# Optimization experiments

Measured on AMD Instinct MI355X. Metric: run time of the kernel, lower is better.

## Reference

```python
import jax, jax.numpy as jnp
import numpy as np

H = 1024
B, S = 8, 2048

def setup_inputs() -> dict:
    key = jax.random.key(0)
    ks = jax.random.split(key, 7)
    inputs = jax.random.normal(ks[0], (B, S, H), dtype=jnp.float32)
    mask = jnp.ones((B, S), dtype=jnp.int32)
    sc = 1.0 / np.sqrt(H)
    Wq = jax.random.normal(ks[1], (H, H), dtype=jnp.float32) * sc
    bq = jnp.zeros((H,), dtype=jnp.float32)
    Wk = jax.random.normal(ks[2], (H, H), dtype=jnp.float32) * sc
    bk = jnp.zeros((H,), dtype=jnp.float32)
    Wv = jax.random.normal(ks[3], (H, H), dtype=jnp.float32) * sc
    bv = jnp.zeros((H,), dtype=jnp.float32)
    return {"inputs": inputs, "mask": mask, "Wq": Wq, "bq": bq, "Wk": Wk, "bk": bk, "Wv": Wv, "bv": bv}

def reference(inputs, mask, Wq, bq, Wk, bk, Wv, bv):
    scale = jnp.asarray(H ** 0.5, inputs.dtype)
    q = jnp.einsum('bsh,hd->bsd', inputs, Wq) + bq
    k = jnp.einsum('bsh,hd->bsd', inputs, Wk) + bk
    v = jnp.einsum('bsh,hd->bsd', inputs, Wv) + bv
    scores = jnp.einsum('bqd,bkd->bqk', q, k) / scale  # [B,S,S]
    scores = jnp.where(mask[:, None, :] == 0, -jnp.inf, scores)
    attn = jax.nn.softmax(scores, axis=-1)
    return jnp.einsum('bqk,bkd->bqd', attn, v)
```

## Files before the change

kernel.cpp:

```cpp
#include <hip/hip_runtime.h>
#include <stdint.h>

#define DEVI __device__ __forceinline__

typedef __bf16 bf16x8 __attribute__((ext_vector_type(8)));
typedef float  floatx4 __attribute__((ext_vector_type(4)));


DEVI unsigned short f2bf(float f) {
  union { float f; uint32_t u; } x; x.f = f;
  return (unsigned short)((x.u + 0x7fffu + ((x.u >> 16) & 1u)) >> 16);
}
DEVI float bf2f(unsigned short s) {
  union { uint32_t u; float f; } x; x.u = ((uint32_t)s) << 16;
  return x.f;
}

__global__ __launch_bounds__(256) void k_prep(
    const float* __restrict__ X, unsigned short* __restrict__ Xb,
    const float* __restrict__ Wq, const float* __restrict__ Wk,
    const float* __restrict__ Wv, unsigned short* __restrict__ Wt,
    float* __restrict__ lvec) {
  __shared__ float tile[64][65];
  int bx = blockIdx.x, t = threadIdx.x;
  if (bx < 16384) {
    int i = bx * 256 + t;
    float4 v = ((const float4*)X)[i];
    ushort4 o;
    o.x = f2bf(v.x); o.y = f2bf(v.y); o.z = f2bf(v.z); o.w = f2bf(v.w);
    ((ushort4*)Xb)[i] = o;
  } else if (bx < 17152) {
    int idx = bx - 16384;
    int sel = idx >> 8, b2 = idx & 255;
    const float* W = sel == 0 ? Wq : (sel == 1 ? Wk : Wv);
    unsigned short* Wo = Wt + ((size_t)sel << 20);
    int h0 = (b2 & 15) * 64, d0 = (b2 >> 4) * 64;
#pragma unroll
    for (int i = 0; i < 16; ++i) {
      int idx2 = i * 256 + t; int r = idx2 >> 6, c = idx2 & 63;
      tile[r][c] = W[(size_t)(h0 + r) * 1024 + d0 + c];
    }
    __syncthreads();
#pragma unroll
    for (int i = 0; i < 16; ++i) {
      int idx2 = i * 256 + t; int r = idx2 >> 6, c = idx2 & 63;
      Wo[(size_t)(d0 + r) * 1024 + h0 + c] = f2bf(tile[c][r]);
    }
  } else {
    float4 z4 = {0.f, 0.f, 0.f, 0.f};
#pragma unroll
    for (int i = 0; i < 16; ++i) ((float4*)lvec)[i * 256 + t] = z4;
  }
}

DEVI void gl_lds16(const unsigned short* gp, unsigned short* lp) {
  __builtin_amdgcn_global_load_lds(
      (const __attribute__((address_space(1))) void*)gp,
      (__attribute__((address_space(3))) void*)lp, 16, 0, 0);
}

template <int EPI>
__global__ __launch_bounds__(256) void k_gemm(
    const unsigned short* __restrict__ A, const unsigned short* __restrict__ Bt,
    void* __restrict__ Cv,
    const float* __restrict__ bias_q, const float* __restrict__ bias_k,
    const float* __restrict__ bias_v,
    const float* __restrict__ lvec, float* __restrict__ lsum,
    const int* __restrict__ mask,
    long aZ, long bZ, int ldA, int ldB, int kIters)
{
  __shared__ unsigned short As[128 * 64];
  __shared__ unsigned short Bs[128 * 64];
  const int t = threadIdx.x, w = t >> 6, l = t & 63;
  const int quad = l >> 4, l15 = l & 15;
  const int m0 = blockIdx.x * 128;
  const int z = blockIdx.z;
  const int wm = (w & 1) * 64, wn = (w >> 1) * 64;

  int n0, sel = 0;
  if constexpr (EPI == 4) { sel = blockIdx.y >> 3; n0 = (blockIdx.y & 7) * 128; }
  else n0 = blockIdx.y * 128;

  const unsigned short* Az = A + (size_t)z * aZ;
  const unsigned short* Bz = (EPI == 4) ? (Bt + ((size_t)sel << 20))
                                        : (Bt + (size_t)z * bZ);

  floatx4 acc[4][4];
#pragma unroll
  for (int i = 0; i < 4; ++i)
#pragma unroll
    for (int j = 0; j < 4; ++j) { floatx4 zz = {0.f, 0.f, 0.f, 0.f}; acc[i][j] = zz; }

  for (int kt = 0; kt < kIters; ++kt) {
    __syncthreads();
#pragma unroll
    for (int i = 0; i < 4; ++i) {
      int u   = (i * 4 + w) * 64 + l;
      int row = u >> 3;
      int cc  = (u & 7) ^ (row & 7);
      gl_lds16(Az + (size_t)(m0 + row) * ldA + kt * 64 + cc * 8,
               &As[(i * 4 + w) * 512]);
      gl_lds16(Bz + (size_t)(n0 + row) * ldB + kt * 64 + cc * 8,
               &Bs[(i * 4 + w) * 512]);
    }
    __syncthreads();
#pragma unroll
    for (int ks = 0; ks < 2; ++ks) {
      bf16x8 af[4], bfr[4];
#pragma unroll
      for (int ms = 0; ms < 4; ++ms) {
        int r  = wm + ms * 16 + l15;
        int cc = (ks * 4 + quad) ^ (r & 7);
        af[ms] = *(const bf16x8*)&As[r * 64 + cc * 8];
      }
#pragma unroll
      for (int ns = 0; ns < 4; ++ns) {
        int r  = wn + ns * 16 + l15;
        int cc = (ks * 4 + quad) ^ (r & 7);
        bfr[ns] = *(const bf16x8*)&Bs[r * 64 + cc * 8];
      }
#pragma unroll
      for (int ms = 0; ms < 4; ++ms)
#pragma unroll
        for (int ns = 0; ns < 4; ++ns)
          acc[ms][ns] = __builtin_amdgcn_mfma_f32_16x16x32_bf16(
              af[ms], bfr[ns], acc[ms][ns], 0, 0, 0);
    }
  }

  if constexpr (EPI == 4) {
    unsigned short* C = (unsigned short*)Cv + ((size_t)sel << 24);
    const float* bs = sel == 0 ? bias_q : (sel == 1 ? bias_k : bias_v);
    if (sel < 2) {
      float sc = sel == 0 ? 0.03125f : 1.0f;
#pragma unroll
      for (int ns = 0; ns < 4; ++ns) {
        int n_g = n0 + wn + ns * 16 + l15;
        float bv = bs[n_g];
#pragma unroll
        for (int ms = 0; ms < 4; ++ms) {
          int mb = m0 + wm + ms * 16 + quad * 4;
#pragma unroll
          for (int r = 0; r < 4; ++r)
            C[(size_t)(mb + r) * 1024 + n_g] = f2bf((acc[ms][ns][r] + bv) * sc);
        }
      }
    } else {
#pragma unroll
      for (int ns = 0; ns < 4; ++ns) {
        int n_g = n0 + wn + ns * 16 + l15;
        float bv = bs[n_g];
#pragma unroll
        for (int ms = 0; ms < 4; ++ms) {
          int m_g = m0 + wm + ms * 16 + quad * 4;
          int bb = m_g >> 11, key = m_g & 2047;
          ushort4 pk;
          pk.x = f2bf(acc[ms][ns][0] + bv);
          pk.y = f2bf(acc[ms][ns][1] + bv);
          pk.z = f2bf(acc[ms][ns][2] + bv);
          pk.w = f2bf(acc[ms][ns][3] + bv);
          *(ushort4*)&C[((size_t)bb << 21) + ((size_t)n_g << 11) + key] = pk;
        }
      }
    }
  } else if constexpr (EPI == 2) {
    unsigned short* C = (unsigned short*)Cv + (size_t)z * 4194304;
    const int* mz = mask + z * 2048;
    float rowsum[4][4];
#pragma unroll
    for (int ms = 0; ms < 4; ++ms)
#pragma unroll
      for (int r = 0; r < 4; ++r) rowsum[ms][r] = 0.f;
#pragma unroll
    for (int ns = 0; ns < 4; ++ns) {
      int n_g = n0 + wn + ns * 16 + l15;
      int mv = mz[n_g];
#pragma unroll
      for (int ms = 0; ms < 4; ++ms) {
#pragma unroll
        for (int r = 0; r < 4; ++r) {
          int m_g = m0 + wm + ms * 16 + quad * 4 + r;
          float e = mv ? __expf(acc[ms][ns][r]) : 0.f;
          unsigned short pb = f2bf(e);
          C[(size_t)m_g * 2048 + n_g] = pb;
          rowsum[ms][r] += bf2f(pb);
        }
      }
    }
#pragma unroll
    for (int ms = 0; ms < 4; ++ms) {
#pragma unroll
      for (int r = 0; r < 4; ++r) {
        float s = rowsum[ms][r];
#pragma unroll
        for (int off = 1; off < 16; off <<= 1) s += __shfl_xor(s, off);
        if (l15 == 0) {
          int m_g = m0 + wm + ms * 16 + quad * 4 + r;
          atomicAdd(&lsum[z * 2048 + m_g], s);
        }
      }
    }
  } else {
    float* C = (float*)Cv + (size_t)z * 2048 * 1024;
    const float* lz = lvec + z * 2048;
#pragma unroll
    for (int ms = 0; ms < 4; ++ms) {
#pragma unroll
      for (int r = 0; r < 4; ++r) {
        int m_g = m0 + wm + ms * 16 + quad * 4 + r;
        float lw = lz[m_g];
        float inv = lw > 0.f ? 1.f / lw : 0.f;
#pragma unroll
        for (int ns = 0; ns < 4; ++ns) {
          int n_g = n0 + wn + ns * 16 + l15;
          C[(size_t)m_g * 1024 + n_g] = acc[ms][ns][r] * inv;
        }
      }
    }
  }
}

extern "C" void kernel_launch(void* const* d_in, const int* in_sizes, int n_in,
                              void* d_out, int out_size, void* d_ws, size_t ws_size,
                              hipStream_t stream) {
  const float* X    = (const float*)d_in[0];
  const int*   mask = (const int*)d_in[1];
  const float* Wq   = (const float*)d_in[2];
  const float* bq   = (const float*)d_in[3];
  const float* Wk   = (const float*)d_in[4];
  const float* bk   = (const float*)d_in[5];
  const float* Wv   = (const float*)d_in[6];
  const float* bv   = (const float*)d_in[7];
  float* out = (float*)d_out;

  constexpr size_t SZ = (size_t)16384 * 1024;
  unsigned short* Q    = (unsigned short*)d_ws;
  float*          lvec = (float*)(Q + 3 * SZ);
  unsigned short* P    = (unsigned short*)(lvec + 16384);
  unsigned short* Xb   = P;
  unsigned short* Wt   = Xb + SZ;
  unsigned short* Vt   = Q + 2 * SZ;

  k_prep<<<dim3(17153), 256, 0, stream>>>(X, Xb, Wq, Wk, Wv, Wt, lvec);

  k_gemm<4><<<dim3(128, 24, 1), 256, 0, stream>>>(
      Xb, Wt, (void*)Q, bq, bk, bv, nullptr, nullptr, nullptr,
      0, 0, 1024, 1024, 16);

  k_gemm<2><<<dim3(16, 16, 8), 256, 0, stream>>>(
      Q, Q + SZ, (void*)P, nullptr, nullptr, nullptr, nullptr, lvec, mask,
      2048 * 1024, 2048 * 1024, 1024, 1024, 16);

  k_gemm<3><<<dim3(16, 8, 8), 256, 0, stream>>>(
      P, Vt, (void*)out, nullptr, nullptr, nullptr, lvec, nullptr, nullptr,
      2048 * 2048, 1024 * 2048, 2048, 2048, 32);
}
```

Before: 454.0 us.

## Use 256x256 double-buffered GEMM tiles with phased prefetch and 8 waves

Rewrites the shared bf16 GEMM kernel to use 512-thread blocks computing 256x256 output tiles. Each wave now holds a 128x64 accumulator, and the A/B tiles are double-buffered in LDS. The k loop is split into four sub-phases that overlap half-tile global-to-LDS prefetches for the next k steps with MFMA work, using explicit vmcnt waits, barriers and setprio. The aim is to hide global load latency and raise data reuse per LDS byte. In exchange, the 128KB of LDS per block and the larger register footprint limit occupancy, and fewer blocks per launch may underfill the GPU on the PV GEMM.

```diff
diff --git a/kernel.cpp b/kernel.cpp
--- a/kernel.cpp
+++ b/kernel.cpp
@@ -59,8 +59,55 @@
       (__attribute__((address_space(3))) void*)lp, 16, 0, 0);
 }
 
+template <bool ISB>
+DEVI void stage_half(const unsigned short* __restrict__ G, unsigned short* L,
+                     int base, int ld, int kt, int q, int w, int l) {
+#pragma unroll
+  for (int j = 0; j < 2; ++j) {
+    int slot = w * 2 + j;
+    int r0 = ISB ? ((slot >> 2) * 64 + q * 32 + (slot & 3) * 8)
+                 : ((slot >> 3) * 128 + q * 64 + (slot & 7) * 8);
+    int r = r0 + (l >> 3);
+    int u = (l & 7) ^ (r & 7);
+    gl_lds16(G + (size_t)(base + r) * ld + (size_t)kt * 64 + u * 8, L + r0 * 64);
+  }
+}
+
+#define PHASE(MH, NH, WAITSTMT, ...)                                          \
+  do {                                                                        \
+    bf16x8 af[2][4], bfr[2][2];                                               \
+    _Pragma("unroll") for (int kk = 0; kk < 2; ++kk) {                        \
+      _Pragma("unroll") for (int ms = 0; ms < 4; ++ms) {                      \
+        int rr = wm + MH * 64 + ms * 16 + l15;                                \
+        int cc = (kk * 4 + quad) ^ (rr & 7);                                  \
+        af[kk][ms] = *(const bf16x8*)&Ac[rr * 64 + cc * 8];                   \
+      }                                                                       \
+      _Pragma("unroll") for (int ns = 0; ns < 2; ++ns) {                      \
+        int rr = wn + NH * 32 + ns * 16 + l15;                                \
+        int cc = (kk * 4 + quad) ^ (rr & 7);                                  \
+        bfr[kk][ns] = *(const bf16x8*)&Bc[rr * 64 + cc * 8];                  \
+      }                                                                       \
+    }                                                                         \
+    __VA_ARGS__;                                                              \
+    __builtin_amdgcn_s_barrier();                                             \
+    __builtin_amdgcn_s_setprio(1);                                            \
+    _Pragma("unroll") for (int kk = 0; kk < 2; ++kk)                          \
+      _Pragma("unroll") for (int ms = 0; ms < 4; ++ms)                        \
+        _Pragma("unroll") for (int ns = 0; ns < 2; ++ns)                      \
+          acc[MH * 4 + ms][NH * 2 + ns] =                                     \
+              __builtin_amdgcn_mfma_f32_16x16x32_bf16(                        \
+                  af[kk][ms], bfr[kk][ns], acc[MH * 4 + ms][NH * 2 + ns],     \
+                  0, 0, 0);                                                   \
+    __builtin_amdgcn_s_setprio(0);                                            \
+    WAITSTMT;                                                                 \
+    __builtin_amdgcn_s_barrier();                                             \
+  } while (0)
+
+#define WAITV4 asm volatile("s_waitcnt vmcnt(4)" ::: "memory")
+#define WAITV0 asm volatile("s_waitcnt vmcnt(0)" ::: "memory")
+
 template <int EPI>
-__global__ __launch_bounds__(256) void k_gemm(
+__global__ __launch_bounds__(512, 2) void k_gemm(
     const unsigned short* __restrict__ A, const unsigned short* __restrict__ Bt,
     void* __restrict__ Cv,
     const float* __restrict__ bias_q, const float* __restrict__ bias_k,
@@ -69,63 +116,56 @@
     const int* __restrict__ mask,
     long aZ, long bZ, int ldA, int ldB, int kIters)
 {
-  __shared__ unsigned short As[128 * 64];
-  __shared__ unsigned short Bs[128 * 64];
-  const int t = threadIdx.x, w = t >> 6, l = t & 63;
+  __shared__ __attribute__((aligned(16))) unsigned short As[2][256 * 64];
+  __shared__ __attribute__((aligned(16))) unsigned short Bs[2][256 * 64];
+  const int tid = threadIdx.x, w = tid >> 6, l = tid & 63;
   const int quad = l >> 4, l15 = l & 15;
-  const int m0 = blockIdx.x * 128;
+  const int wr = w & 1, wc = w >> 1;
+  const int wm = wr * 128, wn = wc * 64;
+  const int m0 = blockIdx.x * 256;
   const int z = blockIdx.z;
-  const int wm = (w & 1) * 64, wn = (w >> 1) * 64;
 
   int n0, sel = 0;
-  if constexpr (EPI == 4) { sel = blockIdx.y >> 3; n0 = (blockIdx.y & 7) * 128; }
-  else n0 = blockIdx.y * 128;
+  if constexpr (EPI == 4) { sel = blockIdx.y >> 2; n0 = (blockIdx.y & 3) * 256; }
+  else n0 = blockIdx.y * 256;
 
   const unsigned short* Az = A + (size_t)z * aZ;
   const unsigned short* Bz = (EPI == 4) ? (Bt + ((size_t)sel << 20))
                                         : (Bt + (size_t)z * bZ);
 
-  floatx4 acc[4][4];
-#pragma unroll
-  for (int i = 0; i < 4; ++i)
+  floatx4 acc[8][4];
+#pragma unroll
+  for (int i = 0; i < 8; ++i)
 #pragma unroll
     for (int j = 0; j < 4; ++j) { floatx4 zz = {0.f, 0.f, 0.f, 0.f}; acc[i][j] = zz; }
 
+  stage_half<false>(Az, As[0], m0, ldA, 0, 0, w, l);
+  stage_half<true >(Bz, Bs[0], n0, ldB, 0, 0, w, l);
+  stage_half<false>(Az, As[0], m0, ldA, 0, 1, w, l);
+  stage_half<true >(Bz, Bs[0], n0, ldB, 0, 1, w, l);
+  if (kIters > 1) {
+    stage_half<false>(Az, As[1], m0, ldA, 1, 0, w, l);
+    stage_half<true >(Bz, Bs[1], n0, ldB, 1, 0, w, l);
+    WAITV4;
+  } else {
+    WAITV0;
+  }
+  __builtin_amdgcn_s_barrier();
+
+#pragma unroll 2
   for (int kt = 0; kt < kIters; ++kt) {
-    __syncthreads();
-#pragma unroll
-    for (int i = 0; i < 4; ++i) {
-      int u   = (i * 4 + w) * 64 + l;
-      int row = u >> 3;
-      int cc  = (u & 7) ^ (row & 7);
-      gl_lds16(Az + (size_t)(m0 + row) * ldA + kt * 64 + cc * 8,
-               &As[(i * 4 + w) * 512]);
-      gl_lds16(Bz + (size_t)(n0 + row) * ldB + kt * 64 + cc * 8,
-               &Bs[(i * 4 + w) * 512]);
-    }
-    __syncthreads();
-#pragma unroll
-    for (int ks = 0; ks < 2; ++ks) {
-      bf16x8 af[4], bfr[4];
-#pragma unroll
-      for (int ms = 0; ms < 4; ++ms) {
-        int r  = wm + ms * 16 + l15;
-        int cc = (ks * 4 + quad) ^ (r & 7);
-        af[ms] = *(const bf16x8*)&As[r * 64 + cc * 8];
-      }
-#pragma unroll
-      for (int ns = 0; ns < 4; ++ns) {
-        int r  = wn + ns * 16 + l15;
-        int cc = (ks * 4 + quad) ^ (r & 7);
-        bfr[ns] = *(const bf16x8*)&Bs[r * 64 + cc * 8];
-      }
-#pragma unroll
-      for (int ms = 0; ms < 4; ++ms)
-#pragma unroll
-        for (int ns = 0; ns < 4; ++ns)
-          acc[ms][ns] = __builtin_amdgcn_mfma_f32_16x16x32_bf16(
-              af[ms], bfr[ns], acc[ms][ns], 0, 0, 0);
-    }
+    const int bc = kt & 1, bn = bc ^ 1;
+    const unsigned short* Ac = As[bc];
+    const unsigned short* Bc = Bs[bc];
+    PHASE(0, 0, {},
+          if (kt + 1 < kIters) stage_half<false>(Az, As[bn], m0, ldA, kt + 1, 1, w, l));
+    PHASE(0, 1, {},
+          if (kt + 1 < kIters) stage_half<true >(Bz, Bs[bn], n0, ldB, kt + 1, 1, w, l));
+    PHASE(1, 0, {},
+          if (kt + 2 < kIters) stage_half<false>(Az, As[bc], m0, ldA, kt + 2, 0, w, l));
+    PHASE(1, 1,
+          { if (kt + 2 < kIters) { WAITV4; } else { WAITV0; } },
+          if (kt + 2 < kIters) stage_half<true >(Bz, Bs[bc], n0, ldB, kt + 2, 0, w, l));
   }
 
   if constexpr (EPI == 4) {
@@ -138,7 +178,7 @@
         int n_g = n0 + wn + ns * 16 + l15;
         float bv = bs[n_g];
 #pragma unroll
-        for (int ms = 0; ms < 4; ++ms) {
+        for (int ms = 0; ms < 8; ++ms) {
           int mb = m0 + wm + ms * 16 + quad * 4;
 #pragma unroll
           for (int r = 0; r < 4; ++r)
@@ -151,7 +191,7 @@
         int n_g = n0 + wn + ns * 16 + l15;
         float bv = bs[n_g];
 #pragma unroll
-        for (int ms = 0; ms < 4; ++ms) {
+        for (int ms = 0; ms < 8; ++ms) {
           int m_g = m0 + wm + ms * 16 + quad * 4;
           int bb = m_g >> 11, key = m_g & 2047;
           ushort4 pk;
@@ -166,9 +206,9 @@
   } else if constexpr (EPI == 2) {
     unsigned short* C = (unsigned short*)Cv + (size_t)z * 4194304;
     const int* mz = mask + z * 2048;
-    float rowsum[4][4];
-#pragma unroll
-    for (int ms = 0; ms < 4; ++ms)
+    float rowsum[8][4];
+#pragma unroll
+    for (int ms = 0; ms < 8; ++ms)
 #pragma unroll
       for (int r = 0; r < 4; ++r) rowsum[ms][r] = 0.f;
 #pragma unroll
@@ -176,7 +216,7 @@
       int n_g = n0 + wn + ns * 16 + l15;
       int mv = mz[n_g];
 #pragma unroll
-      for (int ms = 0; ms < 4; ++ms) {
+      for (int ms = 0; ms < 8; ++ms) {
 #pragma unroll
         for (int r = 0; r < 4; ++r) {
           int m_g = m0 + wm + ms * 16 + quad * 4 + r;
@@ -188,7 +228,7 @@
       }
     }
 #pragma unroll
-    for (int ms = 0; ms < 4; ++ms) {
+    for (int ms = 0; ms < 8; ++ms) {
 #pragma unroll
       for (int r = 0; r < 4; ++r) {
         float s = rowsum[ms][r];
@@ -204,7 +244,7 @@
     float* C = (float*)Cv + (size_t)z * 2048 * 1024;
     const float* lz = lvec + z * 2048;
 #pragma unroll
-    for (int ms = 0; ms < 4; ++ms) {
+    for (int ms = 0; ms < 8; ++ms) {
 #pragma unroll
       for (int r = 0; r < 4; ++r) {
         int m_g = m0 + wm + ms * 16 + quad * 4 + r;
@@ -243,15 +283,15 @@
 
   k_prep<<<dim3(17153), 256, 0, stream>>>(X, Xb, Wq, Wk, Wv, Wt, lvec);
 
-  k_gemm<4><<<dim3(128, 24, 1), 256, 0, stream>>>(
+  k_gemm<4><<<dim3(64, 12, 1), 512, 0, stream>>>(
       Xb, Wt, (void*)Q, bq, bk, bv, nullptr, nullptr, nullptr,
       0, 0, 1024, 1024, 16);
 
-  k_gemm<2><<<dim3(16, 16, 8), 256, 0, stream>>>(
+  k_gemm<2><<<dim3(8, 8, 8), 512, 0, stream>>>(
       Q, Q + SZ, (void*)P, nullptr, nullptr, nullptr, nullptr, lvec, mask,
       2048 * 1024, 2048 * 1024, 1024, 1024, 16);
 
-  k_gemm<3><<<dim3(16, 8, 8), 256, 0, stream>>>(
+  k_gemm<3><<<dim3(8, 4, 8), 512, 0, stream>>>(
       P, Vt, (void*)out, nullptr, nullptr, nullptr, lvec, nullptr, nullptr,
       2048 * 2048, 1024 * 2048, 2048, 2048, 32);
 }
```

Result: no change. 447.8 us (-1.4%).
